# Optimization experiments

Measured on AMD Instinct MI355X. Metric: run time of the kernel, lower is better.

Reference implementation:

```python
import jax, jax.numpy as jnp
import numpy as np

N_NODES = 100000
N_EDGES = 1600000
HIDDEN = 128
LAYERS = 2


def setup_inputs() -> dict:
    key = jax.random.key(0)
    k1, k2, k3, k4 = jax.random.split(key, 4)
    x = jax.random.normal(k1, (N_NODES, HIDDEN), dtype=jnp.float32)
    edge_index = jax.random.randint(k2, (2, N_EDGES), 0, N_NODES, dtype=jnp.int32)
    # Glorot-ish init for per-layer GCN weights, small bias
    Ws = jax.random.normal(k3, (LAYERS, HIDDEN, HIDDEN), dtype=jnp.float32) / np.sqrt(HIDDEN).astype(np.float32)
    bs = jax.random.normal(k4, (LAYERS, HIDDEN), dtype=jnp.float32) * 0.01
    return {"x": x, "edge_index": edge_index, "Ws": Ws, "bs": bs}


def reference(x, edge_index, Ws, bs):
    # PyG GCNConv with normalize=True, add_self_loops=False:
    #   x' = D^{-1/2} A D^{-1/2} (x W) + b,  deg = in-degree at target (col) nodes
    src = edge_index[0]  # message sources (row)
    dst = edge_index[1]  # message targets (col), aggregation index
    ones = jnp.ones(src.shape[0], dtype=x.dtype)
    deg = jax.ops.segment_sum(ones, dst, num_segments=N_NODES)
    dinv = jnp.where(deg > 0, jax.lax.rsqrt(jnp.maximum(deg, 1.0)), jnp.zeros_like(deg))
    norm = dinv[src] * dinv[dst]  # [E] symmetric edge normalization
    for l in range(Ws.shape[0]):
        h = x @ Ws[l]                                  # [N, D] dense transform
        msg = h[src] * norm[:, None]                   # [E, D] gather + scale
        x = jax.ops.segment_sum(msg, dst, num_segments=N_NODES) + bs[l]
    return x
```

## Files before the change

kernel.cpp:

```cpp
#include <hip/hip_runtime.h>

#define HID 128
#define WFRAG (HID*HID)

typedef __attribute__((ext_vector_type(8))) short bf16x8;
typedef __attribute__((ext_vector_type(4))) float f32x4;

static __device__ __forceinline__ unsigned short f2bf(float f){
  unsigned u = __float_as_uint(f);
  unsigned r = (u + 0x7FFF + ((u >> 16) & 1)) >> 16;
  return (unsigned short)r;
}
static __device__ __forceinline__ float bf2f_lo(unsigned u){ return __uint_as_float(u << 16); }
static __device__ __forceinline__ float bf2f_hi(unsigned u){ return __uint_as_float(u & 0xFFFF0000u); }

static __device__ __forceinline__ unsigned cvtpk(float lo, float hi){
  unsigned r;
  asm volatile("v_cvt_pk_bf16_f32 %0, %1, %2" : "=v"(r) : "v"(lo), "v"(hi));
  return r;
}

__global__ __launch_bounds__(256) void k_wprep(const float* __restrict__ Ws,
                                               unsigned short* __restrict__ Whi,
                                               unsigned short* __restrict__ Wlo){
  int layer = blockIdx.x;
  const float* W = Ws + (size_t)layer*HID*HID;
  for (int idx = threadIdx.x; idx < 2048; idx += 256){
    int lane = idx & 63, kstep = (idx>>6)&3, nblk = idx>>8;
    int col = 16*nblk + (lane&15);
    int k0  = 32*kstep + 8*(lane>>4);
    size_t obase = ((size_t)(layer*8 + nblk)*4 + kstep)*512 + (size_t)lane*8;
    for (int j = 0; j < 8; j++){
      float v = W[(size_t)(k0+j)*HID + col];
      unsigned short h = f2bf(v);
      float hf = __uint_as_float((unsigned)h << 16);
      Whi[obase+j] = h;
      Wlo[obase+j] = f2bf(v - hf);
    }
  }
}

static __device__ __forceinline__ void gemm_body_f32(int bid, const float* __restrict__ X,
                                                     const unsigned short* __restrict__ Whi,
                                                     const unsigned short* __restrict__ Wlo,
                                                     unsigned short* __restrict__ H2u, int N){
  int t = threadIdx.x, w = t>>6, l = t&63;
  int row0 = bid*32;
  int lrow = l & 15, lk = (l>>4)*8;
  f32x4 acc[2][2] = {};
#pragma unroll 1
  for (int kstep = 0; kstep < 4; kstep++){
    bf16x8 ahi[2], alo[2];
#pragma unroll
    for (int m = 0; m < 2; m++){
      int row = row0 + 16*m + lrow;
      if (row >= N) row = N-1;
      const float* ap = X + (size_t)row*HID + kstep*32 + lk;
      float4 a0 = *(const float4*)ap;
      float4 a1 = *(const float4*)(ap+4);
      int4 hh, ll;
      hh.x = cvtpk(a0.x, a0.y); hh.y = cvtpk(a0.z, a0.w);
      hh.z = cvtpk(a1.x, a1.y); hh.w = cvtpk(a1.z, a1.w);
      ll.x = cvtpk(a0.x - bf2f_lo(hh.x), a0.y - bf2f_hi(hh.x));
      ll.y = cvtpk(a0.z - bf2f_lo(hh.y), a0.w - bf2f_hi(hh.y));
      ll.z = cvtpk(a1.x - bf2f_lo(hh.z), a1.y - bf2f_hi(hh.z));
      ll.w = cvtpk(a1.z - bf2f_lo(hh.w), a1.w - bf2f_hi(hh.w));
      ahi[m] = *(bf16x8*)&hh;
      alo[m] = *(bf16x8*)&ll;
    }
#pragma unroll
    for (int n = 0; n < 2; n++){
      size_t base = ((size_t)((2*w+n)*4 + kstep))*512 + (size_t)l*8;
      bf16x8 bhi = *(const bf16x8*)(Whi + base);
      bf16x8 blo = *(const bf16x8*)(Wlo + base);
#pragma unroll
      for (int m = 0; m < 2; m++){
        acc[m][n] = __builtin_amdgcn_mfma_f32_16x16x32_bf16(ahi[m], bhi, acc[m][n], 0, 0, 0);
        acc[m][n] = __builtin_amdgcn_mfma_f32_16x16x32_bf16(alo[m], bhi, acc[m][n], 0, 0, 0);
        acc[m][n] = __builtin_amdgcn_mfma_f32_16x16x32_bf16(ahi[m], blo, acc[m][n], 0, 0, 0);
      }
    }
  }
#pragma unroll
  for (int m = 0; m < 2; m++)
#pragma unroll
    for (int r = 0; r < 4; r++){
      int row = row0 + 16*m + 4*(l>>4) + r;
      if (row < N){
#pragma unroll
        for (int n = 0; n < 2; n++){
          int col = 16*(2*w+n) + lrow;
          H2u[(size_t)row*HID + col] = f2bf(acc[m][n][r]);
        }
      }
    }
}

__global__ __launch_bounds__(256) void k_pos_gemm0(const int* __restrict__ dst, int* __restrict__ fill,
                                                   int* __restrict__ pos, int E, int Gp,
                                                   const unsigned short* __restrict__ Whi,
                                                   const unsigned short* __restrict__ Wlo,
                                                   const float* __restrict__ X,
                                                   unsigned short* __restrict__ H2u, int N){
  int bid = blockIdx.x;
  if (bid < Gp){
    int e = bid*256 + threadIdx.x;
    if (e < E) pos[e] = atomicAdd(&fill[dst[e]], 1);
    return;
  }
  gemm_body_f32(bid - Gp, X, Whi, Wlo, H2u, N);
}

__global__ __launch_bounds__(256) void k_alloc(const int* __restrict__ deg, int* __restrict__ rowstart,
                                               float* __restrict__ dinv, int* __restrict__ cursor, int N){
  __shared__ int sm[256];
  __shared__ int sbase;
  int t = threadIdx.x;
  int n = blockIdx.x*256 + t;
  int d = (n < N) ? deg[n] : 0;
  sm[t] = d;
  __syncthreads();
  for (int off = 1; off < 256; off <<= 1){
    int v = (t >= off) ? sm[t-off] : 0;
    __syncthreads();
    sm[t] += v;
    __syncthreads();
  }
  if (t == 255) sbase = atomicAdd(cursor, sm[255]);
  __syncthreads();
  if (n < N){
    rowstart[n] = sbase + sm[t] - d;
    dinv[n] = d > 0 ? rsqrtf((float)d) : 0.0f;
  }
}

__global__ __launch_bounds__(256) void k_scatter(const int* __restrict__ src, const int* __restrict__ dst,
                                                 const int* __restrict__ pos, const int* __restrict__ rowstart,
                                                 const float* __restrict__ dinv,
                                                 int2* __restrict__ slots, int E){
  int i0 = (blockIdx.x*256 + threadIdx.x)*2;
  if (i0 + 1 < E){
    int2 s = *(const int2*)(src + i0);
    int2 d = *(const int2*)(dst + i0);
    int2 p = *(const int2*)(pos + i0);
    slots[rowstart[d.x] + p.x] = make_int2(s.x, __float_as_int(dinv[s.x]));
    slots[rowstart[d.y] + p.y] = make_int2(s.y, __float_as_int(dinv[s.y]));
  } else if (i0 < E){
    int s = src[i0];
    slots[rowstart[dst[i0]] + pos[i0]] = make_int2(s, __float_as_int(dinv[s]));
  }
}

__global__ __launch_bounds__(256) void k_gemm_bf16(const unsigned short* __restrict__ Xb,
                                                   const unsigned short* __restrict__ Whi,
                                                   const unsigned short* __restrict__ Wlo,
                                                   unsigned short* __restrict__ H2u, int N){
  int t = threadIdx.x, w = t>>6, l = t&63;
  int row0 = blockIdx.x*32;
  int lrow = l & 15, lk = (l>>4)*8;
  f32x4 acc[2][2] = {};
#pragma unroll 1
  for (int kstep = 0; kstep < 4; kstep++){
    bf16x8 a[2];
#pragma unroll
    for (int m = 0; m < 2; m++){
      int row = row0 + 16*m + lrow;
      if (row >= N) row = N-1;
      a[m] = *(const bf16x8*)(Xb + (size_t)row*HID + kstep*32 + lk);
    }
#pragma unroll
    for (int n = 0; n < 2; n++){
      size_t base = ((size_t)((2*w+n)*4 + kstep))*512 + (size_t)l*8;
      bf16x8 bhi = *(const bf16x8*)(Whi + base);
      bf16x8 blo = *(const bf16x8*)(Wlo + base);
#pragma unroll
      for (int m = 0; m < 2; m++){
        acc[m][n] = __builtin_amdgcn_mfma_f32_16x16x32_bf16(a[m], bhi, acc[m][n], 0, 0, 0);
        acc[m][n] = __builtin_amdgcn_mfma_f32_16x16x32_bf16(a[m], blo, acc[m][n], 0, 0, 0);
      }
    }
  }
#pragma unroll
  for (int m = 0; m < 2; m++)
#pragma unroll
    for (int r = 0; r < 4; r++){
      int row = row0 + 16*m + 4*(l>>4) + r;
      if (row < N){
#pragma unroll
        for (int n = 0; n < 2; n++){
          int col = 16*(2*w+n) + lrow;
          H2u[(size_t)row*HID + col] = f2bf(acc[m][n][r]);
        }
      }
    }
}

template<int OUTBF>
__global__ __launch_bounds__(256) void k_agg(const uint4* __restrict__ H4, const int2* __restrict__ slots,
                                             const int* __restrict__ rowstart, const int* __restrict__ deg,
                                             const float* __restrict__ dinv,
                                             const float* __restrict__ bias, void* __restrict__ outp, int N){
  int wid = threadIdx.x >> 6, lane = threadIdx.x & 63;
  int n = blockIdx.x*4 + wid;
  if (n >= N) return;
  int st = rowstart[n], cnt = deg[n];
  int g = lane >> 4, c = lane & 15;
  float a[8] = {0.f,0.f,0.f,0.f,0.f,0.f,0.f,0.f};
  for (int j = 0; j < cnt; j += 16){
    int cl = cnt - 1;
    int2 sl[4];
#pragma unroll
    for (int q = 0; q < 4; q++){
      int jj = j + 4*q + g;
      sl[q] = slots[st + (jj < cnt ? jj : cl)];
    }
    uint4 v[4];
#pragma unroll
    for (int q = 0; q < 4; q++) v[q] = H4[(size_t)sl[q].x*16 + c];
#pragma unroll
    for (int q = 0; q < 4; q++){
      float wq = (j + 4*q + g < cnt) ? __int_as_float(sl[q].y) : 0.f;
      a[0] += wq*bf2f_lo(v[q].x);
      a[1] += wq*bf2f_hi(v[q].x);
      a[2] += wq*bf2f_lo(v[q].y);
      a[3] += wq*bf2f_hi(v[q].y);
      a[4] += wq*bf2f_lo(v[q].z);
      a[5] += wq*bf2f_hi(v[q].z);
      a[6] += wq*bf2f_lo(v[q].w);
      a[7] += wq*bf2f_hi(v[q].w);
    }
  }
#pragma unroll
  for (int q = 0; q < 8; q++){
    a[q] += __shfl_xor(a[q], 16);
    a[q] += __shfl_xor(a[q], 32);
  }
  if (g == 0){
    float dv = dinv[n];
    const float4* b4 = (const float4*)bias;
    float4 b0 = b4[c*2], b1 = b4[c*2+1];
    float o[8];
    o[0]=dv*a[0]+b0.x; o[1]=dv*a[1]+b0.y; o[2]=dv*a[2]+b0.z; o[3]=dv*a[3]+b0.w;
    o[4]=dv*a[4]+b1.x; o[5]=dv*a[5]+b1.y; o[6]=dv*a[6]+b1.z; o[7]=dv*a[7]+b1.w;
    if (OUTBF){
      uint4 p;
      p.x = (unsigned)f2bf(o[0]) | ((unsigned)f2bf(o[1]) << 16);
      p.y = (unsigned)f2bf(o[2]) | ((unsigned)f2bf(o[3]) << 16);
      p.z = (unsigned)f2bf(o[4]) | ((unsigned)f2bf(o[5]) << 16);
      p.w = (unsigned)f2bf(o[6]) | ((unsigned)f2bf(o[7]) << 16);
      ((uint4*)outp)[(size_t)n*16 + c] = p;
    } else {
      float4* orow = (float4*)((float*)outp + (size_t)n*HID);
      orow[c*2]   = make_float4(o[0],o[1],o[2],o[3]);
      orow[c*2+1] = make_float4(o[4],o[5],o[6],o[7]);
    }
  }
}

extern "C" void kernel_launch(void* const* d_in, const int* in_sizes, int n_in,
                              void* d_out, int out_size, void* d_ws, size_t ws_size,
                              hipStream_t stream){
  const float* x  = (const float*)d_in[0];
  const int*   ei = (const int*)d_in[1];
  const float* Ws = (const float*)d_in[2];
  const float* bs = (const float*)d_in[3];
  const int N = in_sizes[0] / HID;
  const int E = in_sizes[1] / 2;
  const int L = in_sizes[2] / (HID*HID);
  const int* src = ei;
  const int* dst = ei + E;
  const int NB = (N + 255)/256;

  char* w = (char*)d_ws;
  int*   fill     = (int*)w;   w += (size_t)N*4;
  int*   cursor   = (int*)w;   w += 16;
  size_t zbytes = (size_t)(w - (char*)d_ws);
  float* dinv     = (float*)w; w += (size_t)N*4;
  int*   rowstart = (int*)w;   w += (size_t)N*4;
  int*   pos      = (int*)w;   w += (size_t)E*4;
  int2*  slots    = (int2*)w;  w += (size_t)E*8 + 64;
  unsigned short* h2u = (unsigned short*)w; w += (size_t)N*HID*2;
  unsigned short* xb1 = (unsigned short*)w; w += (size_t)N*HID*2;
  unsigned short* whi = (unsigned short*)w; w += (size_t)L*WFRAG*2;
  unsigned short* wlo = (unsigned short*)w; w += (size_t)L*WFRAG*2;

  hipMemsetAsync(d_ws, 0, zbytes, stream);

  int Gp = (E + 255)/256;
  int Gs = (E/2 + 255)/256 + 1;
  int Gg = (N + 31)/32;
  int Ga = (N + 3)/4;

  k_wprep    <<<L, 256, 0, stream>>>(Ws, whi, wlo);
  k_pos_gemm0<<<Gp + Gg, 256, 0, stream>>>(dst, fill, pos, E, Gp,
                                           whi, wlo, x, h2u, N);
  k_alloc    <<<NB, 256, 0, stream>>>(fill, rowstart, dinv, cursor, N);
  k_scatter  <<<Gs, 256, 0, stream>>>(src, dst, pos, rowstart, dinv, slots, E);

  k_agg<1><<<Ga, 256, 0, stream>>>((const uint4*)h2u, slots, rowstart, fill,
                                   dinv, bs, (void*)xb1, N);
  k_gemm_bf16<<<Gg, 256, 0, stream>>>(xb1, whi + WFRAG, wlo + WFRAG, h2u, N);
  k_agg<0><<<Ga, 256, 0, stream>>>((const uint4*)h2u, slots, rowstart, fill,
                                   dinv, bs + HID, d_out, N);
}
```

Measured before the change: 331.3 us.

## Privatize degree-count atomics per XCD and fuse layer-0 GEMM with edge scatter

Edge position counting now uses one counter array per XCD, chosen from the hardware XCC id register. Each atomic then stays in that die's local L2 instead of contending across dies. A new allocation kernel sums the per-XCD counts, prefix-scans them and writes per-XCD base offsets. The first GEMM moves from the position kernel into the scatter kernel, so the GEMM overlaps with the scatter rather than with the atomics. The cost is an 8x larger zeroed counter array, an extra xbase array and an extra indirection per edge.

```diff
diff --git a/kernel.cpp b/kernel.cpp
--- a/kernel.cpp
+++ b/kernel.cpp
@@ -2,6 +2,7 @@
 
 #define HID 128
 #define WFRAG (HID*HID)
+#define NXCD 8
 
 typedef __attribute__((ext_vector_type(8))) short bf16x8;
 typedef __attribute__((ext_vector_type(4))) float f32x4;
@@ -40,6 +41,51 @@
   }
 }
 
+__global__ __launch_bounds__(256) void k_pos8(const int* __restrict__ dst, int* __restrict__ fill8,
+                                              int* __restrict__ pos, int E, int N){
+  int xcc = __builtin_amdgcn_s_getreg((31<<11) | 20) & (NXCD-1);
+  int e = blockIdx.x*256 + threadIdx.x;
+  if (e < E){
+    int d = dst[e];
+    int p = atomicAdd(&fill8[(size_t)xcc*N + d], 1);
+    pos[e] = (xcc << 28) | p;
+  }
+}
+
+__global__ __launch_bounds__(256) void k_alloc8(const int* __restrict__ fill8, int* __restrict__ deg,
+                                                int* __restrict__ rowstart, int* __restrict__ xbase,
+                                                float* __restrict__ dinv, int* __restrict__ cursor, int N){
+  __shared__ int sm[256];
+  __shared__ int sbase;
+  int t = threadIdx.x;
+  int n = blockIdx.x*256 + t;
+  int c[NXCD];
+  int d = 0;
+  if (n < N){
+#pragma unroll
+    for (int x = 0; x < NXCD; x++){ c[x] = fill8[(size_t)x*N + n]; d += c[x]; }
+  }
+  sm[t] = d;
+  __syncthreads();
+  for (int off = 1; off < 256; off <<= 1){
+    int v = (t >= off) ? sm[t-off] : 0;
+    __syncthreads();
+    sm[t] += v;
+    __syncthreads();
+  }
+  if (t == 255) sbase = atomicAdd(cursor, sm[255]);
+  __syncthreads();
+  if (n < N){
+    int rs = sbase + sm[t] - d;
+    rowstart[n] = rs;
+    deg[n] = d;
+    dinv[n] = d > 0 ? rsqrtf((float)d) : 0.0f;
+    int xb = rs;
+#pragma unroll
+    for (int x = 0; x < NXCD; x++){ xbase[(size_t)x*N + n] = xb; xb += c[x]; }
+  }
+}
+
 static __device__ __forceinline__ void gemm_body_f32(int bid, const float* __restrict__ X,
                                                      const unsigned short* __restrict__ Whi,
                                                      const unsigned short* __restrict__ Wlo,
@@ -96,58 +142,28 @@
     }
 }
 
-__global__ __launch_bounds__(256) void k_pos_gemm0(const int* __restrict__ dst, int* __restrict__ fill,
-                                                   int* __restrict__ pos, int E, int Gp,
-                                                   const unsigned short* __restrict__ Whi,
-                                                   const unsigned short* __restrict__ Wlo,
-                                                   const float* __restrict__ X,
-                                                   unsigned short* __restrict__ H2u, int N){
+__global__ __launch_bounds__(256) void k_gemm0_scatter(const float* __restrict__ X,
+                                                       const unsigned short* __restrict__ Whi,
+                                                       const unsigned short* __restrict__ Wlo,
+                                                       unsigned short* __restrict__ H2u, int N, int Gg,
+                                                       const int* __restrict__ src, const int* __restrict__ dst,
+                                                       const int* __restrict__ pos, const int* __restrict__ xbase,
+                                                       const float* __restrict__ dinv,
+                                                       int2* __restrict__ slots, int E){
   int bid = blockIdx.x;
-  if (bid < Gp){
-    int e = bid*256 + threadIdx.x;
-    if (e < E) pos[e] = atomicAdd(&fill[dst[e]], 1);
-    return;
-  }
-  gemm_body_f32(bid - Gp, X, Whi, Wlo, H2u, N);
-}
-
-__global__ __launch_bounds__(256) void k_alloc(const int* __restrict__ deg, int* __restrict__ rowstart,
-                                               float* __restrict__ dinv, int* __restrict__ cursor, int N){
-  __shared__ int sm[256];
-  __shared__ int sbase;
-  int t = threadIdx.x;
-  int n = blockIdx.x*256 + t;
-  int d = (n < N) ? deg[n] : 0;
-  sm[t] = d;
-  __syncthreads();
-  for (int off = 1; off < 256; off <<= 1){
-    int v = (t >= off) ? sm[t-off] : 0;
-    __syncthreads();
-    sm[t] += v;
-    __syncthreads();
-  }
-  if (t == 255) sbase = atomicAdd(cursor, sm[255]);
-  __syncthreads();
-  if (n < N){
-    rowstart[n] = sbase + sm[t] - d;
-    dinv[n] = d > 0 ? rsqrtf((float)d) : 0.0f;
-  }
-}
-
-__global__ __launch_bounds__(256) void k_scatter(const int* __restrict__ src, const int* __restrict__ dst,
-                                                 const int* __restrict__ pos, const int* __restrict__ rowstart,
-                                                 const float* __restrict__ dinv,
-                                                 int2* __restrict__ slots, int E){
-  int i0 = (blockIdx.x*256 + threadIdx.x)*2;
+  if (bid < Gg){ gemm_body_f32(bid, X, Whi, Wlo, H2u, N); return; }
+  int i0 = ((bid - Gg)*256 + threadIdx.x)*2;
   if (i0 + 1 < E){
     int2 s = *(const int2*)(src + i0);
     int2 d = *(const int2*)(dst + i0);
     int2 p = *(const int2*)(pos + i0);
-    slots[rowstart[d.x] + p.x] = make_int2(s.x, __float_as_int(dinv[s.x]));
-    slots[rowstart[d.y] + p.y] = make_int2(s.y, __float_as_int(dinv[s.y]));
+    int slot0 = xbase[(size_t)(p.x >> 28)*N + d.x] + (p.x & 0x0FFFFFFF);
+    int slot1 = xbase[(size_t)(p.y >> 28)*N + d.y] + (p.y & 0x0FFFFFFF);
+    slots[slot0] = make_int2(s.x, __float_as_int(dinv[s.x]));
+    slots[slot1] = make_int2(s.y, __float_as_int(dinv[s.y]));
   } else if (i0 < E){
-    int s = src[i0];
-    slots[rowstart[dst[i0]] + pos[i0]] = make_int2(s, __float_as_int(dinv[s]));
+    int s = src[i0], d = dst[i0], p = pos[i0];
+    slots[xbase[(size_t)(p >> 28)*N + d] + (p & 0x0FFFFFFF)] = make_int2(s, __float_as_int(dinv[s]));
   }
 }
 
@@ -272,11 +288,13 @@
   const int NB = (N + 255)/256;
 
   char* w = (char*)d_ws;
-  int*   fill     = (int*)w;   w += (size_t)N*4;
+  int*   fill8    = (int*)w;   w += (size_t)NXCD*N*4;
   int*   cursor   = (int*)w;   w += 16;
   size_t zbytes = (size_t)(w - (char*)d_ws);
+  int*   deg      = (int*)w;   w += (size_t)N*4;
   float* dinv     = (float*)w; w += (size_t)N*4;
   int*   rowstart = (int*)w;   w += (size_t)N*4;
+  int*   xbase    = (int*)w;   w += (size_t)NXCD*N*4;
   int*   pos      = (int*)w;   w += (size_t)E*4;
   int2*  slots    = (int2*)w;  w += (size_t)E*8 + 64;
   unsigned short* h2u = (unsigned short*)w; w += (size_t)N*HID*2;
@@ -291,15 +309,14 @@
   int Gg = (N + 31)/32;
   int Ga = (N + 3)/4;
 
-  k_wprep    <<<L, 256, 0, stream>>>(Ws, whi, wlo);
-  k_pos_gemm0<<<Gp + Gg, 256, 0, stream>>>(dst, fill, pos, E, Gp,
-                                           whi, wlo, x, h2u, N);
-  k_alloc    <<<NB, 256, 0, stream>>>(fill, rowstart, dinv, cursor, N);
-  k_scatter  <<<Gs, 256, 0, stream>>>(src, dst, pos, rowstart, dinv, slots, E);
-
-  k_agg<1><<<Ga, 256, 0, stream>>>((const uint4*)h2u, slots, rowstart, fill,
+  k_wprep <<<L, 256, 0, stream>>>(Ws, whi, wlo);
+  k_pos8  <<<Gp, 256, 0, stream>>>(dst, fill8, pos, E, N);
+  k_alloc8<<<NB, 256, 0, stream>>>(fill8, deg, rowstart, xbase, dinv, cursor, N);
+  k_gemm0_scatter<<<Gg + Gs, 256, 0, stream>>>(x, whi, wlo, h2u, N, Gg,
+                                               src, dst, pos, xbase, dinv, slots, E);
+  k_agg<1><<<Ga, 256, 0, stream>>>((const uint4*)h2u, slots, rowstart, deg,
                                    dinv, bs, (void*)xb1, N);
   k_gemm_bf16<<<Gg, 256, 0, stream>>>(xb1, whi + WFRAG, wlo + WFRAG, h2u, N);
-  k_agg<0><<<Ga, 256, 0, stream>>>((const uint4*)h2u, slots, rowstart, fill,
+  k_agg<0><<<Ga, 256, 0, stream>>>((const uint4*)h2u, slots, rowstart, deg,
                                    dinv, bs + HID, d_out, N);
 }
```

Result: no change. 326.6 us (-1.4%).
